# Kernel optimization log

Measured on AMD Instinct MI355X. Metric: run time of the kernel, lower is better.

The kernel has to match this reference:

```python
import jax, jax.numpy as jnp
import numpy as np

BN_EPS = 1e-5
NORM_EPS = 1e-12  # F.normalize eps
NUM_HEADS = 8
QUERY_DIM = 256
TOP_K = 16


def _l2norm(x):
    n = jnp.linalg.norm(x, axis=-1, keepdims=True)
    return x / jnp.maximum(n, NORM_EPS)


def setup_inputs() -> dict:
    key = jax.random.key(0)
    ks = jax.random.split(key, 8)
    B, S, D, O, N = 2, 512, 1024, 1024, 16384
    return {
        "hidden_states": jax.random.normal(ks[0], (B, S, D), jnp.float32),
        "Wq": jax.random.normal(ks[1], (D, NUM_HEADS * QUERY_DIM), jnp.float32) * 0.02,
        "bq": jnp.zeros((NUM_HEADS * QUERY_DIM,), jnp.float32),
        "bn_gamma": jnp.ones((QUERY_DIM,), jnp.float32),
        "bn_beta": jnp.zeros((QUERY_DIM,), jnp.float32),
        "sub_keys0": jax.random.normal(ks[2], (128, 128), jnp.float32) * 0.02,
        "sub_keys1": jax.random.normal(ks[3], (128, 128), jnp.float32) * 0.02,
        "expert_down": jax.random.normal(ks[4], (N, D), jnp.float32) * 0.02,
        "expert_up": jax.random.normal(ks[5], (N, O), jnp.float32) * 0.02,
    }


def reference(hidden_states, Wq, bq, bn_gamma, bn_beta, sub_keys0, sub_keys1, expert_down, expert_up):
    B, S, D = hidden_states.shape
    H, QD, K = NUM_HEADS, QUERY_DIM, TOP_K

    # query projection -> [B,S,H,QD]
    q = (hidden_states @ Wq + bq).reshape(B, S, H, QD)

    # BatchNorm1d over flattened (B*S*H, QD), training-mode batch stats (biased var)
    qf = q.reshape(-1, QD)
    mean = qf.mean(axis=0)
    var = qf.var(axis=0)
    qf = (qf - mean) * jax.lax.rsqrt(var + BN_EPS) * bn_gamma + bn_beta
    q = qf.reshape(B, S, H, QD)

    # split query into two halves, L2-normalize queries and keys, sub-scores
    half = QD // 2
    s0 = jnp.einsum('bshd,nd->bshn', _l2norm(q[..., :half]), _l2norm(sub_keys0))  # [B,S,H,128]
    s1 = jnp.einsum('bshd,nd->bshn', _l2norm(q[..., half:]), _l2norm(sub_keys1))  # [B,S,H,128]

    # cartesian-product scores: flat expert idx = i*128 + j (matches meshgrid 'ij')
    total = (s0[..., :, None] + s1[..., None, :]).reshape(B, S, H, -1)  # [B,S,H,16384]

    top_scores, top_idx = jax.lax.top_k(total, K)  # [B,S,H,K]
    w = jax.nn.softmax(top_scores, axis=-1)

    dw = expert_down[top_idx]  # [B,S,H,K,D]  (expert_hidden_size = 1)
    uw = expert_up[top_idx]    # [B,S,H,K,O]

    ei = jnp.einsum('bshkd,bsd->bshk', dw, hidden_states)  # per-expert scalar hidden
    eo = jax.nn.gelu(ei, approximate=False)                # F.gelu default = erf
    out = jnp.einsum('bshko,bshk,bshk->bso', uw, eo, w)    # weighted sum over K and H
    return out
```

## Files before the change

kernel.cpp:

```cpp
#include <hip/hip_runtime.h>
#include <math.h>

typedef unsigned long long u64;
typedef unsigned int u32;
typedef unsigned short ushort_t;
typedef _Float16 half8 __attribute__((ext_vector_type(8)));
typedef float f32x4 __attribute__((ext_vector_type(4)));

#define TOKENS 1024
#define DDIM   1024
#define NHEAD  8
#define QD     256
#define HQD    2048
#define NROWS  8192
#define NKEY   128
#define TOPK   16

#define QSCALE 256.0f
#define QINVS  (1.0f / 65536.0f)

__device__ __forceinline__ ushort_t f2bf(float f) {
    u32 u = __float_as_uint(f);
    u32 r = (u + 0x7FFFu + ((u >> 16) & 1u)) >> 16;
    return (ushort_t)r;
}
__device__ __forceinline__ float bf_lo(u32 w) { return __uint_as_float(w << 16); }
__device__ __forceinline__ float bf_hi(u32 w) { return __uint_as_float(w & 0xFFFF0000u); }

__device__ __forceinline__ void hsplit(float x, ushort_t& h, ushort_t& l) {
    _Float16 hh = (_Float16)x;
    float r = x - (float)hh;
    _Float16 ll = (_Float16)r;
    union { _Float16 f; ushort_t u; } c1, c2;
    c1.f = hh; c2.f = ll;
    h = c1.u; l = c2.u;
}

template<int NTHR, int ITERS>
__device__ __forceinline__ void cvt_chunk(int gcb, int tid,
                                          const float* __restrict__ down,
                                          const float* __restrict__ up,
                                          ushort_t* __restrict__ downb,
                                          ushort_t* __restrict__ upb) {
    const float* src = (gcb < 1024) ? down : up;
    ushort_t* dst = (gcb < 1024) ? downb : upb;
    const size_t base4 = (size_t)(gcb & 1023) * 4096;
    const float4* s4 = (const float4*)src;
    ushort4* d4 = (ushort4*)dst;
#pragma unroll 4
    for (int it = 0; it < ITERS; it++) {
        size_t i = base4 + (size_t)it * NTHR + tid;
        float4 v = s4[i];
        ushort4 o;
        o.x = f2bf(v.x); o.y = f2bf(v.y); o.z = f2bf(v.z); o.w = f2bf(v.w);
        d4[i] = o;
    }
}

__global__ __launch_bounds__(256) void k_prep1(
    const float* __restrict__ A, const float* __restrict__ W,
    ushort_t* __restrict__ Ab, ushort_t* __restrict__ Wt,
    const float* __restrict__ sk0, const float* __restrict__ sk1,
    float* __restrict__ k0n, float* __restrict__ k1n)
{
    __shared__ __align__(16) char praw[18464];
    const int bid = blockIdx.x;
    const int tid = threadIdx.x;

    if (bid < 128) {
#pragma unroll
        for (int i = 0; i < 8; i++) {
            const int row = bid * 8 + i;
            float4 v = *(const float4*)(A + (size_t)row * 1024 + tid * 4);
            ushort4 h, l;
            hsplit(v.x * QSCALE, h.x, l.x);
            hsplit(v.y * QSCALE, h.y, l.y);
            hsplit(v.z * QSCALE, h.z, l.z);
            hsplit(v.w * QSCALE, h.w, l.w);
            *(ushort4*)(Ab + (size_t)row * 2048 + tid * 4) = h;
            *(ushort4*)(Ab + (size_t)row * 2048 + 1024 + tid * 4) = l;
        }
    } else if (bid < 640) {
        const int cb = bid - 128;
        const int k0 = (cb >> 5) * 64;
        const int n0 = (cb & 31) * 64;
        ushort_t* Lh = (ushort_t*)praw;
        ushort_t* Ll = (ushort_t*)praw + 4608;
        const int nn = (tid & 15) * 4;
        const int kk = tid >> 4;
#pragma unroll
        for (int p = 0; p < 4; p++) {
            const int k = kk + 16 * p;
            float4 v = *(const float4*)(W + (size_t)(k0 + k) * HQD + n0 + nn);
            float xs[4] = {v.x * QSCALE, v.y * QSCALE, v.z * QSCALE, v.w * QSCALE};
#pragma unroll
            for (int j = 0; j < 4; j++) {
                ushort_t h, l;
                hsplit(xs[j], h, l);
                Lh[(nn + j) * 72 + k] = h;
                Ll[(nn + j) * 72 + k] = l;
            }
        }
        __syncthreads();
#pragma unroll
        for (int e = 0; e < 2; e++) {
            const int idx = tid + 256 * e;
            const int n = idx >> 3, ks = idx & 7;
            uint4 hv = *(const uint4*)(Lh + n * 72 + ks * 8);
            uint4 lv = *(const uint4*)(Ll + n * 72 + ks * 8);
            *(uint4*)(Wt + (size_t)(n0 + n) * 2048 + k0 + ks * 8) = hv;
            *(uint4*)(Wt + (size_t)(n0 + n) * 2048 + 1024 + k0 + ks * 8) = lv;
        }
    } else {
        float* fs = (float*)praw;
        const int b2 = bid - 640;
        const int sub = tid >> 7;
        const int col = tid & 127;
        const int gr = b2 * 2 + sub;
        const float* src = (gr < 128) ? sk0 : sk1;
        float* dst = (gr < 128) ? k0n : k1n;
        const int row = gr & 127;
        float v = src[row * 128 + col];
        float sq = v * v;
        for (int off = 32; off; off >>= 1) sq += __shfl_down(sq, off);
        if ((tid & 63) == 0) fs[tid >> 6] = sq;
        __syncthreads();
        if ((tid & 127) == 0) {
            float n = sqrtf(fs[tid >> 6] + fs[(tid >> 6) + 1]);
            fs[8 + sub] = 1.0f / fmaxf(n, 1e-12f);
        }
        __syncthreads();
        dst[row * 128 + col] = v * fs[8 + sub];
    }
}

__global__ __launch_bounds__(256) void k_fused2(
    const ushort_t* __restrict__ Ab, const ushort_t* __restrict__ Wt,
    float* __restrict__ qp,
    const float* __restrict__ down, const float* __restrict__ up,
    ushort_t* __restrict__ downb, ushort_t* __restrict__ upb)
{
    __shared__ __align__(16) char lds[2][16384];
    const int tid = threadIdx.x;
    const int bid = blockIdx.x;

    if (bid >= 512) {
        cvt_chunk<256, 16>(bid - 512, tid, down, up, downb, upb);
        return;
    }

    const int m0 = (bid >> 5) * 64;
    const int n0 = (bid & 31) * 64;

    const int srow = tid >> 2;
    const int scol = (tid & 3) * 16;
    const int swz = (srow & 7) << 4;

    const int lane = tid & 63;
    const int w = tid >> 6;
    const int wmb = (w >> 1) * 32;
    const int wnb = (w & 1) * 32;
    const int fr = lane & 15;
    const int kg = lane >> 4;
    const int rswz = (fr & 7) << 4;

    f32x4 acc[2][2];
#pragma unroll
    for (int i = 0; i < 2; i++)
#pragma unroll
        for (int j = 0; j < 2; j++)
            acc[i][j] = (f32x4){0.f, 0.f, 0.f, 0.f};

    uint4 ar0, ar1, br0, br1;

    auto LOADR = [&](int gs) {
        const int term = gs >> 4;
        const int aoff = (term == 1) ? 1024 : 0;
        const int woff = (term == 2) ? 1024 : 0;
        const int kb = (gs & 15) * 64;
        const ushort_t* ap = Ab + (size_t)(m0 + srow) * 2048 + aoff + kb + scol;
        const ushort_t* wp = Wt + (size_t)(n0 + srow) * 2048 + woff + kb + scol;
        ar0 = *(const uint4*)(ap);
        ar1 = *(const uint4*)(ap + 8);
        br0 = *(const uint4*)(wp);
        br1 = *(const uint4*)(wp + 8);
    };
    auto WLDS = [&](int buf) {
        char* As = lds[buf];
        char* Bs = lds[buf] + 8192;
        const int b0 = (srow * 128 + scol * 2) ^ swz;
        const int b1 = (srow * 128 + scol * 2 + 16) ^ swz;
        *(uint4*)(As + b0) = ar0;
        *(uint4*)(As + b1) = ar1;
        *(uint4*)(Bs + b0) = br0;
        *(uint4*)(Bs + b1) = br1;
    };

    LOADR(0);
    WLDS(0);

    for (int s = 0; s < 48; s++) {
        __syncthreads();
        if (s < 47) LOADR(s + 1);
        const char* As = lds[s & 1];
        const char* Bs = lds[s & 1] + 8192;
#pragma unroll
        for (int kh = 0; kh < 2; kh++) {
            half8 a[2], b[2];
#pragma unroll
            for (int f = 0; f < 2; f++) {
                const int rowA = wmb + f * 16 + fr;
                a[f] = *(const half8*)(As + ((rowA * 128 + kh * 64 + kg * 16) ^ rswz));
                const int rowB = wnb + f * 16 + fr;
                b[f] = *(const half8*)(Bs + ((rowB * 128 + kh * 64 + kg * 16) ^ rswz));
            }
#pragma unroll
            for (int fm = 0; fm < 2; fm++)
#pragma unroll
                for (int fn = 0; fn < 2; fn++)
                    acc[fm][fn] = __builtin_amdgcn_mfma_f32_16x16x32_f16(
                        a[fm], b[fn], acc[fm][fn], 0, 0, 0);
        }
        if (s < 47) WLDS((s + 1) & 1);
    }

#pragma unroll
    for (int fm = 0; fm < 2; fm++) {
        const int rbase = m0 + wmb + fm * 16 + kg * 4;
#pragma unroll
        for (int fn = 0; fn < 2; fn++) {
            const int c = n0 + wnb + fn * 16 + fr;
#pragma unroll
            for (int j = 0; j < 4; j++)
                qp[(size_t)(rbase + j) * HQD + c] = acc[fm][fn][j];
        }
    }
}

__global__ __launch_bounds__(256) void k_bnstat1(const float* __restrict__ qp,
                                                 const float* __restrict__ bq,
                                                 float* __restrict__ psum,
                                                 float* __restrict__ psq,
                                                 float qsc,
                                                 const float* __restrict__ down,
                                                 const float* __restrict__ up,
                                                 ushort_t* __restrict__ downb,
                                                 ushort_t* __restrict__ upb)
{
    const int b = blockIdx.x;
    const int j = threadIdx.x;
    if (b >= 512) {
        cvt_chunk<256, 16>(512 + (b - 512), j, down, up, downb, upb);
        return;
    }
    float s = 0.f, sq = 0.f;
#pragma unroll 4
    for (int rr = 0; rr < 16; rr++) {
        const int r = b * 16 + rr;
        const size_t g = (size_t)r * 256 + j;
        float v = qp[g] * qsc + bq[(r & 7) * 256 + j];
        s += v; sq += v * v;
    }
    psum[b * 256 + j] = s;
    psq[b * 256 + j]  = sq;
}

__global__ __launch_bounds__(256) void k_bnstat2(const float* __restrict__ psum,
                                                 const float* __restrict__ psq,
                                                 const float* __restrict__ gamma,
                                                 float* __restrict__ meanOut,
                                                 float* __restrict__ scaleOut)
{
    const int j = threadIdx.x;
    float s = 0.f, sq = 0.f;
    for (int b = 0; b < 512; b++) {
        s += psum[b * 256 + j];
        sq += psq[b * 256 + j];
    }
    float mean = s * (1.0f / 8192.0f);
    float var = sq * (1.0f / 8192.0f) - mean * mean;
    meanOut[j] = mean;
    scaleOut[j] = gamma[j] / sqrtf(var + 1e-5f);
}

__global__ __launch_bounds__(256) void k_scores(const float* __restrict__ qp,
                                                const float* __restrict__ bq,
                                                const float* __restrict__ mean,
                                                const float* __restrict__ scale,
                                                const float* __restrict__ beta,
                                                const float* __restrict__ kn0,
                                                const float* __restrict__ kn1,
                                                float* __restrict__ sOut0,
                                                float* __restrict__ sOut1,
                                                float qsc,
                                                const float* __restrict__ down,
                                                const float* __restrict__ up,
                                                ushort_t* __restrict__ downb,
                                                ushort_t* __restrict__ upb)
{
    __shared__ float Qs[128 * 68];
    __shared__ float Ks[64 * 132];
    __shared__ float rp[4][64];
    __shared__ float invn[64];
    const int bid = blockIdx.x;
    const int tid = threadIdx.x;
    if (bid >= 256) {
        cvt_chunk<256, 16>(768 + (bid - 256), tid, down, up, downb, upb);
        return;
    }
    const int half = bid >> 7;
    const int row0 = (bid & 127) * 64;

    {
        const int d4 = (tid & 31) * 4;
        const int rbase = tid >> 5;
        const int j4 = half * 128 + d4;
        float4 m4 = *(const float4*)(mean + j4);
        float4 sc4 = *(const float4*)(scale + j4);
        float4 be4 = *(const float4*)(beta + j4);
        float4 bi4 = *(const float4*)(bq + rbase * 256 + j4);
#pragma unroll
        for (int p = 0; p < 8; p++) {
            const int rr = rbase + p * 8;
            const int row = row0 + rr;
            const size_t g = (size_t)(row >> 3) * 2048 + (size_t)rbase * 256 + j4;
            float4 a = *(const float4*)(qp + g);
            float x0 = (a.x * qsc + bi4.x - m4.x) * sc4.x + be4.x;
            float x1 = (a.y * qsc + bi4.y - m4.y) * sc4.y + be4.y;
            float x2 = (a.z * qsc + bi4.z - m4.z) * sc4.z + be4.z;
            float x3 = (a.w * qsc + bi4.w - m4.w) * sc4.w + be4.w;
            Qs[(d4 + 0) * 68 + rr] = x0;
            Qs[(d4 + 1) * 68 + rr] = x1;
            Qs[(d4 + 2) * 68 + rr] = x2;
            Qs[(d4 + 3) * 68 + rr] = x3;
        }
    }
    __syncthreads();
    {
        const int r = tid & 63, qd = tid >> 6;
        float s = 0.f;
#pragma unroll 8
        for (int d = qd * 32; d < qd * 32 + 32; d++) {
            float v = Qs[d * 68 + r];
            s += v * v;
        }
        rp[qd][r] = s;
    }
    __syncthreads();
    if (tid < 64) {
        float s = rp[0][tid] + rp[1][tid] + rp[2][tid] + rp[3][tid];
        invn[tid] = 1.0f / fmaxf(sqrtf(s), 1e-12f);
    }

    const float* kn = half ? kn1 : kn0;
    float* sOut = half ? sOut1 : sOut0;
    const int ty = tid >> 5;
    const int tx = tid & 31;
    float acc[8][4] = {};

    for (int c = 0; c < 2; c++) {
        __syncthreads();
        {
            int dd4 = (tid & 15) * 4;
            int n = tid >> 4;
#pragma unroll
            for (int p = 0; p < 8; p++) {
                int nn = n + p * 16;
                float4 v = *(const float4*)(kn + nn * 128 + c * 64 + dd4);
                Ks[(dd4 + 0) * 132 + nn] = v.x; Ks[(dd4 + 1) * 132 + nn] = v.y;
                Ks[(dd4 + 2) * 132 + nn] = v.z; Ks[(dd4 + 3) * 132 + nn] = v.w;
            }
        }
        __syncthreads();
#pragma unroll
        for (int d = 0; d < 64; d++) {
            float a[8], b[4];
            *(float4*)(a)     = *(const float4*)&Qs[(c * 64 + d) * 68 + ty * 8];
            *(float4*)(a + 4) = *(const float4*)&Qs[(c * 64 + d) * 68 + ty * 8 + 4];
            *(float4*)(b)     = *(const float4*)&Ks[d * 132 + tx * 4];
#pragma unroll
            for (int i = 0; i < 8; i++)
#pragma unroll
                for (int j = 0; j < 4; j++)
                    acc[i][j] = fmaf(a[i], b[j], acc[i][j]);
        }
    }
#pragma unroll
    for (int i = 0; i < 8; i++) {
        const float iv = invn[ty * 8 + i];
        float4 r;
        r.x = acc[i][0] * iv; r.y = acc[i][1] * iv;
        r.z = acc[i][2] * iv; r.w = acc[i][3] * iv;
        *(float4*)(sOut + (size_t)(row0 + ty * 8 + i) * 128 + tx * 4) = r;
    }
}

__device__ __forceinline__ u64 mkkey(float v, u32 idx) {
    u32 ub = __float_as_uint(v);
    ub = (ub & 0x80000000u) ? ~ub : (ub | 0x80000000u);
    return ((u64)ub << 32) | (u64)(0xFFFFFFFFu - idx);
}
__device__ __forceinline__ float keyval(u64 k) {
    u32 ub = (u32)(k >> 32);
    u32 fb = (ub & 0x80000000u) ? (ub ^ 0x80000000u) : ~ub;
    return __uint_as_float(fb);
}
__device__ __forceinline__ u32 keyidx(u64 k) {
    return 0xFFFFFFFFu - (u32)(k & 0xFFFFFFFFu);
}

__global__ __launch_bounds__(256) void k_topk(const float* __restrict__ s0,
                                              const float* __restrict__ s1,
                                              int* __restrict__ tIdx,
                                              float* __restrict__ tW,
                                              const float* __restrict__ down,
                                              const float* __restrict__ up,
                                              ushort_t* __restrict__ downb,
                                              ushort_t* __restrict__ upb)
{
    __shared__ float shv[4][2][16];
    __shared__ int   shi[4][2][16];
    const int bid = blockIdx.x;
    if (bid >= 2048) {
        cvt_chunk<256, 16>(1024 + (bid - 2048), threadIdx.x, down, up, downb, upb);
        return;
    }
    const int w = threadIdx.x >> 6;
    const int lane = threadIdx.x & 63;
    const int row = bid * 4 + w;

#pragma unroll
    for (int h = 0; h < 2; h++) {
        const float* s = h ? s1 : s0;
        float v0 = s[(size_t)row * 128 + lane];
        float v1 = s[(size_t)row * 128 + 64 + lane];
        u64 k0 = mkkey(v0, (u32)lane);
        u64 k1 = mkkey(v1, (u32)(lane + 64));
        for (int r = 0; r < 16; r++) {
            u64 m = (k0 > k1) ? k0 : k1;
#pragma unroll
            for (int off = 1; off < 64; off <<= 1) {
                u64 o = __shfl_xor(m, off);
                if (o > m) m = o;
            }
            if (k0 == m) k0 = 0;
            if (k1 == m) k1 = 0;
            if (lane == 0) { shv[w][h][r] = keyval(m); shi[w][h][r] = (int)keyidx(m); }
        }
    }

    u64 ck[4];
#pragma unroll
    for (int qq = 0; qq < 4; qq++) {
        int id = lane + 64 * qq;
        int a = id >> 4, b = id & 15;
        float v = shv[w][0][a] + shv[w][1][b];
        u32 idx = (u32)(shi[w][0][a] * 128 + shi[w][1][b]);
        ck[qq] = mkkey(v, idx);
    }
    float winv = 0.f; u32 wini = 0;
    for (int r = 0; r < 16; r++) {
        u64 m = ck[0];
#pragma unroll
        for (int qq = 1; qq < 4; qq++) if (ck[qq] > m) m = ck[qq];
#pragma unroll
        for (int off = 1; off < 64; off <<= 1) {
            u64 o = __shfl_xor(m, off);
            if (o > m) m = o;
        }
#pragma unroll
        for (int qq = 0; qq < 4; qq++) if (ck[qq] == m) ck[qq] = 0;
        if (lane == r) { winv = keyval(m); wini = keyidx(m); }
    }
    float vmax = __shfl(winv, 0);
    if (lane < 16) {
        float e = expf(winv - vmax);
        float ssum = e;
#pragma unroll
        for (int off = 1; off < 16; off <<= 1) ssum += __shfl_xor(ssum, off, 16);
        tW[(size_t)row * 16 + lane] = e / ssum;
        tIdx[(size_t)row * 16 + lane] = (int)wini;
    }
}

__global__ __launch_bounds__(1024) void k_coef_bf(const float* __restrict__ hidden,
                                                  const ushort_t* __restrict__ downb,
                                                  const int* __restrict__ tIdx,
                                                  const float* __restrict__ tW,
                                                  float* __restrict__ coef,
                                                  const float* __restrict__ down,
                                                  const float* __restrict__ up,
                                                  ushort_t* __restrict__ downb2,
                                                  ushort_t* __restrict__ upb)
{
    const int t = blockIdx.x;
    if (t >= 1024) {
        cvt_chunk<1024, 4>(1536 + (t - 1024), threadIdx.x, down, up, downb2, upb);
        return;
    }
    const int wave = threadIdx.x >> 6, lane = threadIdx.x & 63;
    const float* hp = hidden + (size_t)t * 1024;
    float h[16];
    *(float4*)(h + 0)  = *(const float4*)(hp + lane * 8);
    *(float4*)(h + 4)  = *(const float4*)(hp + lane * 8 + 4);
    *(float4*)(h + 8)  = *(const float4*)(hp + 512 + lane * 8);
    *(float4*)(h + 12) = *(const float4*)(hp + 512 + lane * 8 + 4);

#pragma unroll
    for (int g = 0; g < 2; g++) {
        const int pg = wave * 8 + g * 4;
        float s[4];
        uint4 a[4], b[4];
#pragma unroll
        for (int i = 0; i < 4; i++) {
            const int e = tIdx[(size_t)t * 128 + pg + i];
            const uint4* rp = (const uint4*)(downb + (size_t)e * 1024);
            a[i] = rp[lane];
            b[i] = rp[lane + 64];
        }
#pragma unroll
        for (int i = 0; i < 4; i++) {
            float acc = 0.f;
            const u32* aw = (const u32*)&a[i];
            const u32* bw = (const u32*)&b[i];
#pragma unroll
            for (int c = 0; c < 4; c++) {
                acc = fmaf(bf_lo(aw[c]), h[2 * c], acc);
                acc = fmaf(bf_hi(aw[c]), h[2 * c + 1], acc);
                acc = fmaf(bf_lo(bw[c]), h[8 + 2 * c], acc);
                acc = fmaf(bf_hi(bw[c]), h[8 + 2 * c + 1], acc);
            }
            s[i] = acc;
        }
#pragma unroll
        for (int i = 0; i < 4; i++)
#pragma unroll
            for (int off = 1; off < 64; off <<= 1) s[i] += __shfl_xor(s[i], off);
        if (lane < 4) {
            float x = (lane == 0) ? s[0] : (lane == 1) ? s[1] : (lane == 2) ? s[2] : s[3];
            float wv = tW[(size_t)t * 128 + pg + lane];
            float gl = 0.5f * x * (1.0f + erff(x * 0.70710678118654752f));
            coef[(size_t)t * 128 + pg + lane] = wv * gl;
        }
    }
}

__global__ __launch_bounds__(1024) void k_coef_f32(const float* __restrict__ hidden,
                                                   const float* __restrict__ down,
                                                   const int* __restrict__ tIdx,
                                                   const float* __restrict__ tW,
                                                   float* __restrict__ coef)
{
    __shared__ __align__(16) float hs[1024];
    __shared__ int   eidx[128];
    __shared__ float wv[128];
    const int t = blockIdx.x;
    const int tid = threadIdx.x;
    hs[tid] = hidden[(size_t)t * 1024 + tid];
    if (tid < 128) {
        eidx[tid] = tIdx[(size_t)t * 128 + tid];
        wv[tid]   = tW[(size_t)t * 128 + tid];
    }
    __syncthreads();
    const int wave = tid >> 6, lane = tid & 63;
#pragma unroll 2
    for (int i = 0; i < 8; i++) {
        const int p = wave * 8 + i;
        const float4* dp = (const float4*)(down + (size_t)eidx[p] * 1024);
        float sum = 0.f;
#pragma unroll
        for (int c = 0; c < 4; c++) {
            float4 dv = dp[lane + 64 * c];
            float4 hv = *(const float4*)(hs + (lane + 64 * c) * 4);
            sum += dv.x * hv.x + dv.y * hv.y + dv.z * hv.z + dv.w * hv.w;
        }
        for (int off = 32; off; off >>= 1) sum += __shfl_down(sum, off);
        if (lane == 0) {
            float x = sum;
            float g = 0.5f * x * (1.0f + erff(x * 0.70710678118654752f));
            coef[(size_t)t * 128 + p] = wv[p] * g;
        }
    }
}

__global__ __launch_bounds__(256) void k_accum_bf(const ushort_t* __restrict__ upb,
                                                  const int* __restrict__ tIdx,
                                                  const float* __restrict__ coef,
                                                  float* __restrict__ out)
{
    __shared__ float cf[128];
    __shared__ int   ei[128];
    __shared__ float part[512];
    const int t = blockIdx.x >> 1;
    const int jh = blockIdx.x & 1;
    const int tid = threadIdx.x;
    if (tid < 128) {
        cf[tid] = coef[(size_t)t * 128 + tid];
        ei[tid] = tIdx[(size_t)t * 128 + tid];
    }
    __syncthreads();
    const int half = tid >> 7;
    const int jl = (tid & 127) * 4;
    const int j4 = jh * 512 + jl;
    float acc[4] = {};
    const int p0 = half * 64;
#pragma unroll 16
    for (int p = p0; p < p0 + 64; p++) {
        const float c = cf[p];
        uint2 v = *(const uint2*)(upb + (size_t)ei[p] * 1024 + j4);
        acc[0] = fmaf(c, bf_lo(v.x), acc[0]);
        acc[1] = fmaf(c, bf_hi(v.x), acc[1]);
        acc[2] = fmaf(c, bf_lo(v.y), acc[2]);
        acc[3] = fmaf(c, bf_hi(v.y), acc[3]);
    }
    if (half == 0) *(float4*)&part[jl] = *(float4*)acc;
    __syncthreads();
    if (half == 1) {
        float4 pv = *(float4*)&part[jl];
        float4 r;
        r.x = acc[0] + pv.x; r.y = acc[1] + pv.y;
        r.z = acc[2] + pv.z; r.w = acc[3] + pv.w;
        *(float4*)(out + (size_t)t * 1024 + j4) = r;
    }
}

__global__ __launch_bounds__(256) void k_accum_f32(const float* __restrict__ up,
                                                   const int* __restrict__ tIdx,
                                                   const float* __restrict__ coef,
                                                   float* __restrict__ out)
{
    __shared__ float cf[128];
    __shared__ int   ei[128];
    const int t = blockIdx.x >> 2;
    const int c = blockIdx.x & 3;
    const int tid = threadIdx.x;
    if (tid < 128) {
        cf[tid] = coef[(size_t)t * 128 + tid];
        ei[tid] = tIdx[(size_t)t * 128 + tid];
    }
    __syncthreads();
    const int j = c * 256 + tid;
    float acc = 0.f;
#pragma unroll 8
    for (int p = 0; p < 128; p++)
        acc = fmaf(cf[p], up[(size_t)ei[p] * 1024 + j], acc);
    out[(size_t)t * 1024 + j] = acc;
}

__global__ __launch_bounds__(256) void k_fall1(
    const float* __restrict__ A, const float* __restrict__ W,
    float* __restrict__ qp,
    const float* __restrict__ sk0, const float* __restrict__ sk1,
    float* __restrict__ k0n, float* __restrict__ k1n)
{
    __shared__ float smem[2 * 32 * 68];
    const int bid = blockIdx.x;
    const int tid = threadIdx.x;

    if (bid < 512) {
        float* As = smem;
        float* Bs = smem + 32 * 68;
        const int m0 = (bid >> 5) * 64;
        const int n0 = (bid & 31) * 64;
        const int aM  = tid >> 3;
        const int aK4 = (tid & 7) * 4;
        const int bK  = tid >> 4;
        const int bN4 = (tid & 15) * 4;
        const int ty  = tid >> 4;
        const int tx  = tid & 15;
        float acc[4][4] = {};
        for (int kk = 0; kk < 1024; kk += 32) {
            __syncthreads();
#pragma unroll
            for (int p = 0; p < 2; p++) {
                int m = aM + 32 * p;
                float4 v = *(const float4*)(A + (size_t)(m0 + m) * DDIM + kk + aK4);
                As[(aK4 + 0) * 68 + m] = v.x; As[(aK4 + 1) * 68 + m] = v.y;
                As[(aK4 + 2) * 68 + m] = v.z; As[(aK4 + 3) * 68 + m] = v.w;
            }
#pragma unroll
            for (int p = 0; p < 2; p++) {
                int k = bK + 16 * p;
                float4 v = *(const float4*)(W + (size_t)(kk + k) * HQD + n0 + bN4);
                *(float4*)&Bs[k * 68 + bN4] = v;
            }
            __syncthreads();
#pragma unroll
            for (int k = 0; k < 32; k++) {
                float a[4], b[4];
                *(float4*)(a) = *(const float4*)&As[k * 68 + ty * 4];
                *(float4*)(b) = *(const float4*)&Bs[k * 68 + tx * 4];
#pragma unroll
                for (int i = 0; i < 4; i++)
#pragma unroll
                    for (int j = 0; j < 4; j++)
                        acc[i][j] = fmaf(a[i], b[j], acc[i][j]);
            }
        }
#pragma unroll
        for (int i = 0; i < 4; i++) {
            int m = m0 + ty * 4 + i;
            float4 r;
            r.x = acc[i][0]; r.y = acc[i][1]; r.z = acc[i][2]; r.w = acc[i][3];
            *(float4*)(qp + (size_t)m * HQD + n0 + tx * 4) = r;
        }
    } else {
        const int b2 = bid - 512;
        const int sub = tid >> 7;
        const int col = tid & 127;
        const int gr = b2 * 2 + sub;
        const float* src = (gr < 128) ? sk0 : sk1;
        float* dst = (gr < 128) ? k0n : k1n;
        const int row = gr & 127;
        float v = src[row * 128 + col];
        float sq = v * v;
        for (int off = 32; off; off >>= 1) sq += __shfl_down(sq, off);
        if ((tid & 63) == 0) smem[tid >> 6] = sq;
        __syncthreads();
        if ((tid & 127) == 0) {
            float n = sqrtf(smem[tid >> 6] + smem[(tid >> 6) + 1]);
            smem[8 + sub] = 1.0f / fmaxf(n, 1e-12f);
        }
        __syncthreads();
        dst[row * 128 + col] = v * smem[8 + sub];
    }
}

extern "C" void kernel_launch(void* const* d_in, const int* in_sizes, int n_in,
                              void* d_out, int out_size, void* d_ws, size_t ws_size,
                              hipStream_t stream)
{
    const float* hidden = (const float*)d_in[0];
    const float* Wq     = (const float*)d_in[1];
    const float* bq     = (const float*)d_in[2];
    const float* gamma  = (const float*)d_in[3];
    const float* beta   = (const float*)d_in[4];
    const float* sk0    = (const float*)d_in[5];
    const float* sk1    = (const float*)d_in[6];
    const float* down   = (const float*)d_in[7];
    const float* up     = (const float*)d_in[8];
    float* out = (float*)d_out;

    float* ws = (float*)d_ws;
    size_t o = 0;
    float* qp    = ws + o; o += (size_t)TOKENS * HQD;
    float* ps    = ws + o; o += 512 * 256;
    float* pq    = ws + o; o += 512 * 256;
    float* meanb = ws + o; o += 256;
    float* scaleb= ws + o; o += 256;
    float* k0n   = ws + o; o += NKEY * 128;
    float* k1n   = ws + o; o += NKEY * 128;
    float* s0    = ws + o; o += (size_t)NROWS * 128;
    float* s1    = ws + o; o += (size_t)NROWS * 128;
    float* tW    = ws + o; o += (size_t)NROWS * TOPK;
    int*   tIdx  = (int*)(ws + o); o += (size_t)NROWS * TOPK;
    float* coef  = ws + o; o += (size_t)TOKENS * 128;
    ushort_t* downb = (ushort_t*)(ws + o); o += (size_t)16384 * 1024 / 2;
    ushort_t* upb   = (ushort_t*)(ws + o); o += (size_t)16384 * 1024 / 2;
    ushort_t* Ab    = (ushort_t*)(ws + o); o += (size_t)1024 * 2048 / 2;
    ushort_t* Wt    = (ushort_t*)(ws + o); o += (size_t)2048 * 2048 / 2;
    const int useBF = (ws_size >= o * sizeof(float)) ? 1 : 0;
    const float qsc = useBF ? QINVS : 1.0f;

    if (useBF) {
        k_prep1 <<<768, 256, 0, stream>>>(hidden, Wq, Ab, Wt, sk0, sk1, k0n, k1n);
        k_fused2<<<1024, 256, 0, stream>>>(Ab, Wt, qp, down, up, downb, upb);
        k_bnstat1<<<768, 256, 0, stream>>>(qp, bq, ps, pq, qsc, down, up, downb, upb);
        k_bnstat2<<<1, 256, 0, stream>>>(ps, pq, gamma, meanb, scaleb);
        k_scores <<<512, 256, 0, stream>>>(qp, bq, meanb, scaleb, beta,
                                           k0n, k1n, s0, s1, qsc,
                                           down, up, downb, upb);
        k_topk   <<<2560, 256, 0, stream>>>(s0, s1, tIdx, tW, down, up, downb, upb);
        k_coef_bf<<<1536, 1024, 0, stream>>>(hidden, downb, tIdx, tW, coef,
                                             down, up, downb, upb);
        k_accum_bf<<<2048, 256, 0, stream>>>(upb, tIdx, coef, out);
    } else {
        k_fall1 <<<640, 256, 0, stream>>>(hidden, Wq, qp, sk0, sk1, k0n, k1n);
        k_bnstat1<<<512, 256, 0, stream>>>(qp, bq, ps, pq, qsc, down, up, downb, upb);
        k_bnstat2<<<1, 256, 0, stream>>>(ps, pq, gamma, meanb, scaleb);
        k_scores <<<256, 256, 0, stream>>>(qp, bq, meanb, scaleb, beta,
                                           k0n, k1n, s0, s1, qsc,
                                           down, up, downb, upb);
        k_topk   <<<2048, 256, 0, stream>>>(s0, s1, tIdx, tW, down, up, downb, upb);
        k_coef_f32 <<<TOKENS, 1024, 0, stream>>>(hidden, down, tIdx, tW, coef);
        k_accum_f32<<<4096, 256, 0, stream>>>(up, tIdx, coef, out);
    }
}
```

Baseline: 222.1 us.

## Replace iterative shuffle top-k with ballot radix-select and parallelize BN stats reduction

```diff
diff --git a/kernel.cpp b/kernel.cpp
--- a/kernel.cpp
+++ b/kernel.cpp
@@ -34,6 +34,14 @@
     union { _Float16 f; ushort_t u; } c1, c2;
     c1.f = hh; c2.f = ll;
     h = c1.u; l = c2.u;
+}
+
+__device__ __forceinline__ u32 ordf(float v) {
+    u32 u = __float_as_uint(v);
+    return (u & 0x80000000u) ? ~u : (u | 0x80000000u);
+}
+__device__ __forceinline__ u64 mkkey2(float v, u32 idx) {
+    return ((u64)ordf(v) << 32) | (u64)(0xFFFFFFFFu - idx);
 }
 
 template<int NTHR, int ITERS>
@@ -271,16 +279,29 @@
                                                  float* __restrict__ meanOut,
                                                  float* __restrict__ scaleOut)
 {
-    const int j = threadIdx.x;
+    __shared__ float ls[8][64];
+    const int col = blockIdx.x * 32 + (threadIdx.x & 31);
+    const int seg = threadIdx.x >> 5;
     float s = 0.f, sq = 0.f;
-    for (int b = 0; b < 512; b++) {
-        s += psum[b * 256 + j];
-        sq += psq[b * 256 + j];
-    }
-    float mean = s * (1.0f / 8192.0f);
-    float var = sq * (1.0f / 8192.0f) - mean * mean;
-    meanOut[j] = mean;
-    scaleOut[j] = gamma[j] / sqrtf(var + 1e-5f);
+    for (int b = seg; b < 512; b += 8) {
+        s += psum[b * 256 + col];
+        sq += psq[b * 256 + col];
+    }
+    ls[seg][(threadIdx.x & 31)] = s;
+    ls[seg][32 + (threadIdx.x & 31)] = sq;
+    __syncthreads();
+    if (threadIdx.x < 32) {
+        float ts = 0.f, tq = 0.f;
+#pragma unroll
+        for (int g = 0; g < 8; g++) {
+            ts += ls[g][threadIdx.x];
+            tq += ls[g][32 + threadIdx.x];
+        }
+        float mean = ts * (1.0f / 8192.0f);
+        float var = tq * (1.0f / 8192.0f) - mean * mean;
+        meanOut[col] = mean;
+        scaleOut[col] = gamma[col] / sqrtf(var + 1e-5f);
+    }
 }
 
 __global__ __launch_bounds__(256) void k_scores(const float* __restrict__ qp,
@@ -395,20 +416,6 @@
     }
 }
 
-__device__ __forceinline__ u64 mkkey(float v, u32 idx) {
-    u32 ub = __float_as_uint(v);
-    ub = (ub & 0x80000000u) ? ~ub : (ub | 0x80000000u);
-    return ((u64)ub << 32) | (u64)(0xFFFFFFFFu - idx);
-}
-__device__ __forceinline__ float keyval(u64 k) {
-    u32 ub = (u32)(k >> 32);
-    u32 fb = (ub & 0x80000000u) ? (ub ^ 0x80000000u) : ~ub;
-    return __uint_as_float(fb);
-}
-__device__ __forceinline__ u32 keyidx(u64 k) {
-    return 0xFFFFFFFFu - (u32)(k & 0xFFFFFFFFu);
-}
-
 __global__ __launch_bounds__(256) void k_topk(const float* __restrict__ s0,
                                               const float* __restrict__ s1,
                                               int* __restrict__ tIdx,
@@ -420,6 +427,8 @@
 {
     __shared__ float shv[4][2][16];
     __shared__ int   shi[4][2][16];
+    __shared__ float swv[4][16];
+    __shared__ u32   swi[4][16];
     const int bid = blockIdx.x;
     if (bid >= 2048) {
         cvt_chunk<256, 16>(1024 + (bid - 2048), threadIdx.x, down, up, downb, upb);
@@ -428,58 +437,121 @@
     const int w = threadIdx.x >> 6;
     const int lane = threadIdx.x & 63;
     const int row = bid * 4 + w;
-
+    const u64 below = (1ULL << lane) - 1;
+
+    float v0[2], v1[2];
+    u32 o0[2], o1[2], cur[2];
+    v0[0] = s0[(size_t)row * 128 + lane];
+    v1[0] = s0[(size_t)row * 128 + 64 + lane];
+    v0[1] = s1[(size_t)row * 128 + lane];
+    v1[1] = s1[(size_t)row * 128 + 64 + lane];
 #pragma unroll
     for (int h = 0; h < 2; h++) {
-        const float* s = h ? s1 : s0;
-        float v0 = s[(size_t)row * 128 + lane];
-        float v1 = s[(size_t)row * 128 + 64 + lane];
-        u64 k0 = mkkey(v0, (u32)lane);
-        u64 k1 = mkkey(v1, (u32)(lane + 64));
-        for (int r = 0; r < 16; r++) {
-            u64 m = (k0 > k1) ? k0 : k1;
-#pragma unroll
-            for (int off = 1; off < 64; off <<= 1) {
-                u64 o = __shfl_xor(m, off);
-                if (o > m) m = o;
-            }
-            if (k0 == m) k0 = 0;
-            if (k1 == m) k1 = 0;
-            if (lane == 0) { shv[w][h][r] = keyval(m); shi[w][h][r] = (int)keyidx(m); }
-        }
-    }
-
-    u64 ck[4];
+        o0[h] = ordf(v0[h]); o1[h] = ordf(v1[h]); cur[h] = 0u;
+    }
+    for (int bit = 31; bit >= 0; --bit) {
+#pragma unroll
+        for (int h = 0; h < 2; h++) {
+            u32 cand = cur[h] | (1u << bit);
+            int c = __popcll(__ballot(o0[h] >= cand)) + __popcll(__ballot(o1[h] >= cand));
+            if (c >= 16) cur[h] = cand;
+        }
+    }
+#pragma unroll
+    for (int h = 0; h < 2; h++) {
+        u64 g0 = __ballot(o0[h] > cur[h]);
+        u64 g1 = __ballot(o1[h] > cur[h]);
+        const int cg0 = __popcll(g0);
+        const int cntGT = cg0 + __popcll(g1);
+        const int need = 16 - cntGT;
+        u64 e0 = __ballot(o0[h] == cur[h]);
+        u64 e1 = __ballot(o1[h] == cur[h]);
+        const int ce0 = __popcll(e0);
+        if (o0[h] > cur[h]) {
+            int sl = __popcll(g0 & below);
+            shv[w][h][sl] = v0[h]; shi[w][h][sl] = lane;
+        }
+        if (o1[h] > cur[h]) {
+            int sl = cg0 + __popcll(g1 & below);
+            shv[w][h][sl] = v1[h]; shi[w][h][sl] = lane + 64;
+        }
+        if (o0[h] == cur[h]) {
+            int r = __popcll(e0 & below);
+            if (r < need) { shv[w][h][cntGT + r] = v0[h]; shi[w][h][cntGT + r] = lane; }
+        }
+        if (o1[h] == cur[h]) {
+            int r = ce0 + __popcll(e1 & below);
+            if (r < need) { shv[w][h][cntGT + r] = v1[h]; shi[w][h][cntGT + r] = lane + 64; }
+        }
+    }
+
+    float cv[4]; u32 ci[4], co[4];
 #pragma unroll
     for (int qq = 0; qq < 4; qq++) {
         int id = lane + 64 * qq;
         int a = id >> 4, b = id & 15;
-        float v = shv[w][0][a] + shv[w][1][b];
-        u32 idx = (u32)(shi[w][0][a] * 128 + shi[w][1][b]);
-        ck[qq] = mkkey(v, idx);
-    }
-    float winv = 0.f; u32 wini = 0;
-    for (int r = 0; r < 16; r++) {
-        u64 m = ck[0];
-#pragma unroll
-        for (int qq = 1; qq < 4; qq++) if (ck[qq] > m) m = ck[qq];
-#pragma unroll
-        for (int off = 1; off < 64; off <<= 1) {
-            u64 o = __shfl_xor(m, off);
-            if (o > m) m = o;
-        }
-#pragma unroll
-        for (int qq = 0; qq < 4; qq++) if (ck[qq] == m) ck[qq] = 0;
-        if (lane == r) { winv = keyval(m); wini = keyidx(m); }
-    }
-    float vmax = __shfl(winv, 0);
+        cv[qq] = shv[w][0][a] + shv[w][1][b];
+        ci[qq] = (u32)(shi[w][0][a] * 128 + shi[w][1][b]);
+        co[qq] = ordf(cv[qq]);
+    }
+    u32 curV = 0;
+    for (int bit = 31; bit >= 0; --bit) {
+        u32 cand = curV | (1u << bit);
+        int c = 0;
+#pragma unroll
+        for (int qq = 0; qq < 4; qq++) c += __popcll(__ballot(co[qq] >= cand));
+        if (c >= 16) curV = cand;
+    }
+    bool gtf[4], eqf[4];
+    int cntGT = 0;
+#pragma unroll
+    for (int qq = 0; qq < 4; qq++) {
+        gtf[qq] = (co[qq] > curV);
+        eqf[qq] = (co[qq] == curV);
+        cntGT += __popcll(__ballot(gtf[qq]));
+    }
+    const int need = 16 - cntGT;
+    u32 I = 0;
+    for (int bit = 13; bit >= 0; --bit) {
+        u32 cand = I | ((1u << bit) - 1u);
+        int c = 0;
+#pragma unroll
+        for (int qq = 0; qq < 4; qq++)
+            c += __popcll(__ballot(eqf[qq] && (ci[qq] <= cand)));
+        if (c < need) I |= (1u << bit);
+    }
+    int pre = 0;
+#pragma unroll
+    for (int qq = 0; qq < 4; qq++) {
+        bool sel = gtf[qq] || (eqf[qq] && (ci[qq] <= I));
+        u64 sm = __ballot(sel);
+        if (sel) {
+            int sl = pre + __popcll(sm & below);
+            swv[w][sl] = cv[qq]; swi[w][sl] = ci[qq];
+        }
+        pre += __popcll(sm);
+    }
+
     if (lane < 16) {
-        float e = expf(winv - vmax);
+        float myv = swv[w][lane];
+        u32 myi = swi[w][lane];
+        u64 myk = mkkey2(myv, myi);
+        int rank = 0;
+#pragma unroll
+        for (int j = 0; j < 16; j++) {
+            u64 kj = mkkey2(swv[w][j], swi[w][j]);
+            rank += (kj > myk);
+        }
+        float vmax = myv;
+#pragma unroll
+        for (int off = 1; off < 16; off <<= 1)
+            vmax = fmaxf(vmax, __shfl_xor(vmax, off, 16));
+        float e = expf(myv - vmax);
         float ssum = e;
 #pragma unroll
         for (int off = 1; off < 16; off <<= 1) ssum += __shfl_xor(ssum, off, 16);
-        tW[(size_t)row * 16 + lane] = e / ssum;
-        tIdx[(size_t)row * 16 + lane] = (int)wini;
+        tW[(size_t)row * 16 + rank] = e / ssum;
+        tIdx[(size_t)row * 16 + rank] = (int)myi;
     }
 }
 
@@ -766,7 +838,7 @@
         k_prep1 <<<768, 256, 0, stream>>>(hidden, Wq, Ab, Wt, sk0, sk1, k0n, k1n);
         k_fused2<<<1024, 256, 0, stream>>>(Ab, Wt, qp, down, up, downb, upb);
         k_bnstat1<<<768, 256, 0, stream>>>(qp, bq, ps, pq, qsc, down, up, downb, upb);
-        k_bnstat2<<<1, 256, 0, stream>>>(ps, pq, gamma, meanb, scaleb);
+        k_bnstat2<<<8, 256, 0, stream>>>(ps, pq, gamma, meanb, scaleb);
         k_scores <<<512, 256, 0, stream>>>(qp, bq, meanb, scaleb, beta,
                                            k0n, k1n, s0, s1, qsc,
                                            down, up, downb, upb);
@@ -777,7 +849,7 @@
     } else {
         k_fall1 <<<640, 256, 0, stream>>>(hidden, Wq, qp, sk0, sk1, k0n, k1n);
         k_bnstat1<<<512, 256, 0, stream>>>(qp, bq, ps, pq, qsc, down, up, downb, upb);
-        k_bnstat2<<<1, 256, 0, stream>>>(ps, pq, gamma, meanb, scaleb);
+        k_bnstat2<<<8, 256, 0, stream>>>(ps, pq, gamma, meanb, scaleb);
         k_scores <<<256, 256, 0, stream>>>(qp, bq, meanb, scaleb, beta,
                                            k0n, k1n, s0, s1, qsc,
                                            down, up, downb, upb);
```

Result: faster. 183.3 us (-17.4%).
